# Performance work log

Measured on AMD Instinct MI355X. Metric: run time of the kernel, lower is better.

The kernel has to match this reference:

```python
import jax, jax.numpy as jnp
import numpy as np

BATCH_K = 4  # matches init_kwargs batch_k
B, D = 8192, 128

def setup_inputs() -> dict:
    key = jax.random.key(0)
    x = jax.random.normal(key, (B, D), dtype=jnp.float32)
    return {"x": x}

def _losses(x):
    b = x.shape[0]
    k = BATCH_K
    # Pairwise squared distances via Gram matrix: d2[i,j] = ||x_i - x_j||^2
    sq = jnp.sum(x * x, axis=-1)                      # [B]
    d2 = sq[:, None] + sq[None, :] - 2.0 * (x @ x.T)  # [B, B]
    g = jnp.arange(b) // k                            # group id per row
    same = g[:, None] == g[None, :]
    homo_mask = same & ~jnp.eye(b, dtype=bool)        # same group, i != j
    heter_mask = g[:, None] < g[None, :]              # anchor group strictly before j's group
    cnt_homo = jnp.asarray((b // k) * k * (k - 1), dtype=x.dtype)
    cnt_heter = jnp.sum(heter_mask).astype(x.dtype)
    loss_homo = jnp.sum(jnp.where(homo_mask, d2, 0.0)) / cnt_homo
    loss_heter = jnp.sum(jnp.where(heter_mask, jnp.maximum(1.0 - d2, 0.0), 0.0)) / cnt_heter
    return loss_homo, loss_heter

def reference(x):
    return _losses(x)
```

## Files before the change

### kernel.cpp

```cpp
#include <hip/hip_runtime.h>


#define DIM   128
#define NBT   64
#define NTRI  2080
#define NPREP 512

typedef __bf16 bf16x8 __attribute__((ext_vector_type(8)));
typedef float  f32x16 __attribute__((ext_vector_type(16)));

__device__ __forceinline__ unsigned short f2bf(float f) {
  unsigned int u = __float_as_uint(f);
  u += 0x7fffu + ((u >> 16) & 1u);
  return (unsigned short)(u >> 16);
}

__device__ __forceinline__ float wave_reduce(float v) {
#pragma unroll
  for (int off = 32; off > 0; off >>= 1) v += __shfl_xor(v, off);
  return v;
}

__device__ __forceinline__ void load_lds16(const void* g, void* l) {
  __builtin_amdgcn_global_load_lds(
      (const __attribute__((address_space(1))) void*)g,
      (__attribute__((address_space(3))) void*)l, 16, 0, 0);
}

__global__ __launch_bounds__(256) void prep_kernel(
    const float* __restrict__ x, unsigned short* __restrict__ xb,
    float* __restrict__ sq, float* __restrict__ homo_part) {
  const int wave = threadIdx.x >> 6;
  const int lane = threadIdx.x & 63;
  const int g = blockIdx.x * 4 + wave;
  float s0 = 0.f, s1 = 0.f, q = 0.f;
#pragma unroll
  for (int r = 0; r < 4; ++r) {
    const int row = g * 4 + r;
    const float v0 = x[row * DIM + lane];
    const float v1 = x[row * DIM + lane + 64];
    s0 += v0; s1 += v1;
    float rq = wave_reduce(v0 * v0 + v1 * v1);
    if (lane == 0) sq[row] = rq;
    q += rq;
  }
  float ss = wave_reduce(s0 * s0 + s1 * s1);
  __shared__ float hred[4];
  if (lane == 0) hred[wave] = 8.f * q - 2.f * ss;

  const int r = lane >> 4, s = lane & 15;
  const int row = g * 4 + r;
  const int c = s ^ (row & 15);
  const float4* px = (const float4*)(x + row * DIM + c * 8);
  const float4 u0 = px[0], u1 = px[1];
  unsigned int p0 = (unsigned)f2bf(u0.x) | ((unsigned)f2bf(u0.y) << 16);
  unsigned int p1 = (unsigned)f2bf(u0.z) | ((unsigned)f2bf(u0.w) << 16);
  unsigned int p2 = (unsigned)f2bf(u1.x) | ((unsigned)f2bf(u1.y) << 16);
  unsigned int p3 = (unsigned)f2bf(u1.z) | ((unsigned)f2bf(u1.w) << 16);
  uint4 pk; pk.x = p0; pk.y = p1; pk.z = p2; pk.w = p3;
  *(uint4*)(xb + row * DIM + s * 8) = pk;

  __syncthreads();
  if (threadIdx.x == 0)
    homo_part[blockIdx.x] = hred[0] + hred[1] + hred[2] + hred[3];
}

template<bool DIAG>
__device__ __forceinline__ float epilogue(const f32x16 (&acc)[2][2],
                                          const float* __restrict__ sq,
                                          int r0, int c0, int lc, int lk,
                                          float cj0, float cj1) {
  float hs = 0.f;
#pragma unroll
  for (int fi = 0; fi < 2; ++fi) {
#pragma unroll
    for (int r = 0; r < 16; ++r) {
      const int io = fi * 32 + (r & 3) + 8 * (r >> 2) + 4 * lk;
      const float si = sq[r0 + io];
#pragma unroll
      for (int fj = 0; fj < 2; ++fj) {
        if (DIAG && fi > fj) continue;
        float h = fmaxf(fmaf(2.f, acc[fi][fj][r], (fj ? cj1 : cj0) - si), 0.f);
        if (DIAG && fi == fj) {
          const int i = r0 + io;
          const int j = c0 + fj * 32 + lc;
          if (!((i >> 2) < (j >> 2))) h = 0.f;
        }
        hs += h;
      }
    }
  }
  return hs;
}

__global__ __launch_bounds__(256) void heter_kernel(
    const unsigned short* __restrict__ xb, const float* __restrict__ sq,
    float* __restrict__ partial) {
  __shared__ unsigned short ldsA[128 * DIM];
  __shared__ unsigned short ldsB[128 * DIM];

  const int t = (blockIdx.x & 7) * (NTRI / 8) + (blockIdx.x >> 3);
  int bi = (int)((129.0f - sqrtf(16641.0f - 8.0f * (float)t)) * 0.5f);
  bi = min(max(bi, 0), NBT - 1);
  while ((bi + 1) * NBT - ((bi + 1) * bi) / 2 <= t) ++bi;
  while (bi * NBT - (bi * (bi - 1)) / 2 > t) --bi;
  const int bj = bi + (t - (bi * NBT - (bi * (bi - 1)) / 2));

  const int wave = threadIdx.x >> 6;
  const int lane = threadIdx.x & 63;

  const unsigned short* gA = xb + bi * 128 * DIM;
  const unsigned short* gB = xb + bj * 128 * DIM;
#pragma unroll
  for (int i = 0; i < 8; ++i) {
    const int e = (wave * 32 + i * 4) * DIM;
    load_lds16(gA + e + lane * 8, &ldsA[e]);
    load_lds16(gB + e + lane * 8, &ldsB[e]);
  }
  __syncthreads();

  const int wi = wave >> 1, wj = wave & 1;
  const int lc = lane & 31;
  const int lk = lane >> 5;
  const bool diagBlock = (bi == bj);

  float hs = 0.f;
  if (!(diagBlock && wj < wi)) {
    const int ra = (wi * 64 + lc) * DIM;
    const int rb = (wj * 64 + lc) * DIM;
    const int sl = lc & 15;

    f32x16 acc[2][2];
#pragma unroll
    for (int a = 0; a < 2; ++a)
#pragma unroll
      for (int b = 0; b < 2; ++b)
#pragma unroll
        for (int v = 0; v < 16; ++v) acc[a][b][v] = 0.f;

#pragma unroll
    for (int ks = 0; ks < 8; ++ks) {
      const int so = ((ks * 2 + lk) ^ sl) * 8;
      bf16x8 a0 = *(const bf16x8*)&ldsA[ra + so];
      bf16x8 a1 = *(const bf16x8*)&ldsA[ra + 32 * DIM + so];
      bf16x8 b0 = *(const bf16x8*)&ldsB[rb + so];
      bf16x8 b1 = *(const bf16x8*)&ldsB[rb + 32 * DIM + so];
      acc[0][0] = __builtin_amdgcn_mfma_f32_32x32x16_bf16(a0, b0, acc[0][0], 0, 0, 0);
      acc[0][1] = __builtin_amdgcn_mfma_f32_32x32x16_bf16(a0, b1, acc[0][1], 0, 0, 0);
      acc[1][0] = __builtin_amdgcn_mfma_f32_32x32x16_bf16(a1, b0, acc[1][0], 0, 0, 0);
      acc[1][1] = __builtin_amdgcn_mfma_f32_32x32x16_bf16(a1, b1, acc[1][1], 0, 0, 0);
    }

    const int r0 = bi * 128 + wi * 64;
    const int c0 = bj * 128 + wj * 64;
    const float cj0 = 1.f - sq[c0 + lc];
    const float cj1 = 1.f - sq[c0 + 32 + lc];
    const bool diagWave = diagBlock && (wi == wj);
    hs = diagWave ? epilogue<true>(acc, sq, r0, c0, lc, lk, cj0, cj1)
                  : epilogue<false>(acc, sq, r0, c0, lc, lk, cj0, cj1);
  }

  hs = wave_reduce(hs);
  __shared__ float red[4];
  if (lane == 0) red[wave] = hs;
  __syncthreads();
  if (threadIdx.x == 0) partial[t] = red[0] + red[1] + red[2] + red[3];
}

__global__ __launch_bounds__(256) void finalize_kernel(
    const float* __restrict__ partial, const float* __restrict__ homo_part,
    float* __restrict__ out) {
  float s = 0.f, hmo = 0.f;
  for (int i = threadIdx.x; i < NTRI; i += 256) s += partial[i];
  for (int i = threadIdx.x; i < NPREP; i += 256) hmo += homo_part[i];
  s = wave_reduce(s);
  hmo = wave_reduce(hmo);
  __shared__ float red[4], hred[4];
  const int wave = threadIdx.x >> 6, lane = threadIdx.x & 63;
  if (lane == 0) { red[wave] = s; hred[wave] = hmo; }
  __syncthreads();
  if (threadIdx.x == 0) {
    out[0] = (hred[0] + hred[1] + hred[2] + hred[3]) / 24576.f;
    out[1] = (red[0] + red[1] + red[2] + red[3]) / 33538048.f;
  }
}

extern "C" void kernel_launch(void* const* d_in, const int* in_sizes, int n_in,
                              void* d_out, int out_size, void* d_ws, size_t ws_size,
                              hipStream_t stream) {
  const float* x = (const float*)d_in[0];
  float* out = (float*)d_out;
  char* ws = (char*)d_ws;
  float* homo_part   = (float*)(ws);
  float* partial     = (float*)(ws + 2048);
  float* sq          = (float*)(ws + 10496);
  unsigned short* xb = (unsigned short*)(ws + 43264);

  hipLaunchKernelGGL(prep_kernel, dim3(NPREP), dim3(256), 0, stream, x, xb, sq, homo_part);
  hipLaunchKernelGGL(heter_kernel, dim3(NTRI), dim3(256), 0, stream, xb, sq, partial);
  hipLaunchKernelGGL(finalize_kernel, dim3(1), dim3(256), 0, stream, partial, homo_part, out);
}
```

Measured before the change: 78.76 us.

## Enlarge heter tiles to 256x256 with 512-thread blocks and shared diagonal loads

```diff
diff --git a/kernel.cpp b/kernel.cpp
--- a/kernel.cpp
+++ b/kernel.cpp
@@ -2,8 +2,8 @@
 
 
 #define DIM   128
-#define NBT   64
-#define NTRI  2080
+#define NBT   32
+#define NTRI  528
 #define NPREP 512
 
 typedef __bf16 bf16x8 __attribute__((ext_vector_type(8)));
@@ -65,42 +65,14 @@
     homo_part[blockIdx.x] = hred[0] + hred[1] + hred[2] + hred[3];
 }
 
-template<bool DIAG>
-__device__ __forceinline__ float epilogue(const f32x16 (&acc)[2][2],
-                                          const float* __restrict__ sq,
-                                          int r0, int c0, int lc, int lk,
-                                          float cj0, float cj1) {
-  float hs = 0.f;
-#pragma unroll
-  for (int fi = 0; fi < 2; ++fi) {
-#pragma unroll
-    for (int r = 0; r < 16; ++r) {
-      const int io = fi * 32 + (r & 3) + 8 * (r >> 2) + 4 * lk;
-      const float si = sq[r0 + io];
-#pragma unroll
-      for (int fj = 0; fj < 2; ++fj) {
-        if (DIAG && fi > fj) continue;
-        float h = fmaxf(fmaf(2.f, acc[fi][fj][r], (fj ? cj1 : cj0) - si), 0.f);
-        if (DIAG && fi == fj) {
-          const int i = r0 + io;
-          const int j = c0 + fj * 32 + lc;
-          if (!((i >> 2) < (j >> 2))) h = 0.f;
-        }
-        hs += h;
-      }
-    }
-  }
-  return hs;
-}
-
-__global__ __launch_bounds__(256) void heter_kernel(
+__global__ __launch_bounds__(512, 2) void heter_kernel(
     const unsigned short* __restrict__ xb, const float* __restrict__ sq,
     float* __restrict__ partial) {
-  __shared__ unsigned short ldsA[128 * DIM];
-  __shared__ unsigned short ldsB[128 * DIM];
+  __shared__ unsigned short ldsA[256 * DIM];
+  __shared__ unsigned short ldsB[256 * DIM];
 
   const int t = (blockIdx.x & 7) * (NTRI / 8) + (blockIdx.x >> 3);
-  int bi = (int)((129.0f - sqrtf(16641.0f - 8.0f * (float)t)) * 0.5f);
+  int bi = (int)((65.0f - sqrtf(4225.0f - 8.0f * (float)t)) * 0.5f);
   bi = min(max(bi, 0), NBT - 1);
   while ((bi + 1) * NBT - ((bi + 1) * bi) / 2 <= t) ++bi;
   while (bi * NBT - (bi * (bi - 1)) / 2 > t) --bi;
@@ -108,31 +80,29 @@
 
   const int wave = threadIdx.x >> 6;
   const int lane = threadIdx.x & 63;
-
-  const unsigned short* gA = xb + bi * 128 * DIM;
-  const unsigned short* gB = xb + bj * 128 * DIM;
+  const bool diagBlock = (bi == bj);
+
+  const unsigned short* gA = xb + bi * 256 * DIM;
+  const unsigned short* gB = xb + bj * 256 * DIM;
 #pragma unroll
   for (int i = 0; i < 8; ++i) {
     const int e = (wave * 32 + i * 4) * DIM;
     load_lds16(gA + e + lane * 8, &ldsA[e]);
-    load_lds16(gB + e + lane * 8, &ldsB[e]);
-  }
-  __syncthreads();
-
-  const int wi = wave >> 1, wj = wave & 1;
+    if (!diagBlock) load_lds16(gB + e + lane * 8, &ldsB[e]);
+  }
+  __syncthreads();
+  const unsigned short* ldsBr = diagBlock ? ldsA : ldsB;
+
+  const int wi = wave >> 2, wj = wave & 3;
   const int lc = lane & 31;
   const int lk = lane >> 5;
-  const bool diagBlock = (bi == bj);
+  const int sl = lc & 15;
 
   float hs = 0.f;
-  if (!(diagBlock && wj < wi)) {
-    const int ra = (wi * 64 + lc) * DIM;
-    const int rb = (wj * 64 + lc) * DIM;
-    const int sl = lc & 15;
-
-    f32x16 acc[2][2];
-#pragma unroll
-    for (int a = 0; a < 2; ++a)
+  if (!(diagBlock && (wj + 1) * 64 <= wi * 128)) {
+    f32x16 acc[4][2];
+#pragma unroll
+    for (int a = 0; a < 4; ++a)
 #pragma unroll
       for (int b = 0; b < 2; ++b)
 #pragma unroll
@@ -141,30 +111,59 @@
 #pragma unroll
     for (int ks = 0; ks < 8; ++ks) {
       const int so = ((ks * 2 + lk) ^ sl) * 8;
-      bf16x8 a0 = *(const bf16x8*)&ldsA[ra + so];
-      bf16x8 a1 = *(const bf16x8*)&ldsA[ra + 32 * DIM + so];
-      bf16x8 b0 = *(const bf16x8*)&ldsB[rb + so];
-      bf16x8 b1 = *(const bf16x8*)&ldsB[rb + 32 * DIM + so];
+      bf16x8 a0 = *(const bf16x8*)&ldsA[(wi * 128 +  0 + lc) * DIM + so];
+      bf16x8 a1 = *(const bf16x8*)&ldsA[(wi * 128 + 32 + lc) * DIM + so];
+      bf16x8 a2 = *(const bf16x8*)&ldsA[(wi * 128 + 64 + lc) * DIM + so];
+      bf16x8 a3 = *(const bf16x8*)&ldsA[(wi * 128 + 96 + lc) * DIM + so];
+      bf16x8 b0 = *(const bf16x8*)&ldsBr[(wj * 64 +  0 + lc) * DIM + so];
+      bf16x8 b1 = *(const bf16x8*)&ldsBr[(wj * 64 + 32 + lc) * DIM + so];
       acc[0][0] = __builtin_amdgcn_mfma_f32_32x32x16_bf16(a0, b0, acc[0][0], 0, 0, 0);
       acc[0][1] = __builtin_amdgcn_mfma_f32_32x32x16_bf16(a0, b1, acc[0][1], 0, 0, 0);
       acc[1][0] = __builtin_amdgcn_mfma_f32_32x32x16_bf16(a1, b0, acc[1][0], 0, 0, 0);
       acc[1][1] = __builtin_amdgcn_mfma_f32_32x32x16_bf16(a1, b1, acc[1][1], 0, 0, 0);
+      acc[2][0] = __builtin_amdgcn_mfma_f32_32x32x16_bf16(a2, b0, acc[2][0], 0, 0, 0);
+      acc[2][1] = __builtin_amdgcn_mfma_f32_32x32x16_bf16(a2, b1, acc[2][1], 0, 0, 0);
+      acc[3][0] = __builtin_amdgcn_mfma_f32_32x32x16_bf16(a3, b0, acc[3][0], 0, 0, 0);
+      acc[3][1] = __builtin_amdgcn_mfma_f32_32x32x16_bf16(a3, b1, acc[3][1], 0, 0, 0);
     }
 
-    const int r0 = bi * 128 + wi * 64;
-    const int c0 = bj * 128 + wj * 64;
-    const float cj0 = 1.f - sq[c0 + lc];
-    const float cj1 = 1.f - sq[c0 + 32 + lc];
-    const bool diagWave = diagBlock && (wi == wj);
-    hs = diagWave ? epilogue<true>(acc, sq, r0, c0, lc, lk, cj0, cj1)
-                  : epilogue<false>(acc, sq, r0, c0, lc, lk, cj0, cj1);
+    const int rbase = bi * 256 + wi * 128;
+    const int cbase = bj * 256 + wj * 64;
+    float cj0 = 1.f - sq[cbase + lc];
+    float cj1 = 1.f - sq[cbase + 32 + lc];
+#pragma unroll
+    for (int fi = 0; fi < 4; ++fi) {
+      const int frow = wi * 128 + fi * 32;
+#pragma unroll
+      for (int r = 0; r < 16; ++r) {
+        const int io = (r & 3) + 8 * (r >> 2) + 4 * lk;
+        const int i = rbase + fi * 32 + io;
+        const float si = sq[i];
+#pragma unroll
+        for (int fj = 0; fj < 2; ++fj) {
+          const int fcol = wj * 64 + fj * 32;
+          if (diagBlock && fcol < frow) continue;
+          float h = fmaxf(fmaf(2.f, acc[fi][fj][r], (fj ? cj1 : cj0) - si), 0.f);
+          if (diagBlock && fcol == frow) {
+            const int j = cbase + fj * 32 + lc;
+            if (!((i >> 2) < (j >> 2))) h = 0.f;
+          }
+          hs += h;
+        }
+      }
+    }
   }
 
   hs = wave_reduce(hs);
-  __shared__ float red[4];
+  __shared__ float red[8];
   if (lane == 0) red[wave] = hs;
   __syncthreads();
-  if (threadIdx.x == 0) partial[t] = red[0] + red[1] + red[2] + red[3];
+  if (threadIdx.x == 0) {
+    float bsum = 0.f;
+#pragma unroll
+    for (int w = 0; w < 8; ++w) bsum += red[w];
+    partial[t] = bsum;
+  }
 }
 
 __global__ __launch_bounds__(256) void finalize_kernel(
@@ -197,6 +196,6 @@
   unsigned short* xb = (unsigned short*)(ws + 43264);
 
   hipLaunchKernelGGL(prep_kernel, dim3(NPREP), dim3(256), 0, stream, x, xb, sq, homo_part);
-  hipLaunchKernelGGL(heter_kernel, dim3(NTRI), dim3(256), 0, stream, xb, sq, partial);
+  hipLaunchKernelGGL(heter_kernel, dim3(NTRI), dim3(512), 0, stream, xb, sq, partial);
   hipLaunchKernelGGL(finalize_kernel, dim3(1), dim3(256), 0, stream, partial, homo_part, out);
 }
```

Result: slower. 96.98 us (+23.1%).
